# Performance work log

Measured on AMD Instinct MI355X. Metric: run time of the kernel, lower is better.

Reference implementation:

```python
import jax, jax.numpy as jnp
import numpy as np

OUTPUT_SIZE = 16384          # number of map units (must be a perfect square)
SIDE = 128.0                 # sqrt(OUTPUT_SIZE)
SIGMA = 2.0                  # neighbourhood std-dev (non-trainable weight in original)
B, D = 2048, 256


def setup_inputs() -> dict:
    key = jax.random.key(0)
    k1, k2 = jax.random.split(key)
    x = jax.random.normal(k1, (B, D), dtype=jnp.float32)
    kernel = jax.random.normal(k2, (D, OUTPUT_SIZE), dtype=jnp.float32) * 0.1
    return {"x": x, "kernel": kernel}


def _grid_coords():
    # 2D coordinates of each flattened map unit: unit k -> (k // side, k % side)
    idx = jnp.arange(OUTPUT_SIZE, dtype=jnp.float32)
    return jnp.floor(idx / SIDE), jnp.mod(idx, SIDE)  # each (size,)


def reference(x, kernel):
    # Squared Euclidean distance of every sample to every prototype: (B, size).
    # Same math as tf.norm(x[:, :, None] - kernel[None])**2, expressed as a GEMM.
    norms2 = (jnp.sum(x * x, axis=1, keepdims=True)
              - 2.0 * (x @ kernel)
              + jnp.sum(kernel * kernel, axis=0, keepdims=True))
    norms2 = jnp.maximum(norms2, 0.0)

    # Winner-take-all unit per sample, mapped to 2D grid coordinates.
    wta = jnp.argmin(norms2, axis=1).astype(jnp.float32)        # (B,)
    mean_r = jnp.floor(wta / SIDE)                               # (B,)
    mean_c = jnp.mod(wta, SIDE)                                  # (B,)

    # Gaussian neighbourhood over the 2D grid, flattened: (B, size).
    gr, gc = _grid_coords()
    dr = gr[None, :] - mean_r[:, None]
    dc = gc[None, :] - mean_c[:, None]
    radials = jnp.exp(-0.5 / (SIGMA * SIGMA) * (dr * dr + dc * dc))

    return radials * norms2
```

## Files before the change

### kernel.cpp

```cpp
#include <hip/hip_runtime.h>
#include <hip/hip_fp16.h>

#define OUTN 16384
#define BATCH 2048
#define DIM   256

typedef _Float16 half8 __attribute__((ext_vector_type(8)));
typedef float    floatx4 __attribute__((ext_vector_type(4)));
typedef unsigned long long u64;

__device__ __forceinline__ void gl2lds16(const void* g, void* l) {
    __builtin_amdgcn_global_load_lds(
        (const __attribute__((address_space(1))) void*)g,
        (__attribute__((address_space(3))) void*)l, 16, 0, 0);
}

__device__ __forceinline__ u64 packkey(float v, int col) {
    unsigned u = __float_as_uint(v);
    u = (u & 0x80000000u) ? ~u : (u | 0x80000000u);
    return ((u64)u << 32) | (unsigned)col;
}
__device__ __forceinline__ float unpackval(u64 p) {
    unsigned u = (unsigned)(p >> 32);
    u = (u & 0x80000000u) ? (u & 0x7fffffffu) : ~u;
    return __uint_as_float(u);
}

__global__ __launch_bounds__(256) void prep_all(
        const float* __restrict__ x, const float* __restrict__ kern,
        _Float16* __restrict__ xh, float* __restrict__ rown,
        _Float16* __restrict__ kT, float* __restrict__ colnp) {
    int blk = blockIdx.x, t = threadIdx.x;
    if (blk < 512) {
        __shared__ float tile[64][65];
        __shared__ float npart[4][64];
        int tx = t & 63, ty = t >> 6;
        int j0 = (blk >> 1) * 64;
        int dhalf = blk & 1, dbase = dhalf * 128;
        float nrm = 0.f;
        for (int pc = 0; pc < 2; pc++) {
            int dc = dbase + pc * 64;
            __syncthreads();
            for (int it = 0; it < 16; it++) {
                int d = dc + ty + it * 4;
                float v = kern[(size_t)d * OUTN + j0 + tx];
                tile[ty + it * 4][tx] = v;
                nrm = fmaf(v, v, nrm);
            }
            __syncthreads();
            for (int c = t; c < 512; c += 256) {
                int j = c >> 3, o8 = (c & 7) * 8;
                half8 h;
                for (int u = 0; u < 8; u++) h[u] = (_Float16)tile[o8 + u][j];
                *(half8*)&kT[(size_t)(j0 + j) * DIM + dc + o8] = h;
            }
        }
        npart[ty][tx] = nrm;
        __syncthreads();
        if (t < 64)
            colnp[(size_t)dhalf * OUTN + j0 + t] =
                npart[0][t] + npart[1][t] + npart[2][t] + npart[3][t];
    } else {
        int b = blk - 512;
        float v = x[b * DIM + t];
        xh[b * DIM + t] = (_Float16)v;
        float s = v * v;
        for (int off = 32; off; off >>= 1) s += __shfl_down(s, off, 64);
        __shared__ float wsum[4];
        if ((t & 63) == 0) wsum[t >> 6] = s;
        __syncthreads();
        if (t == 0) rown[b] = wsum[0] + wsum[1] + wsum[2] + wsum[3];
    }
}

template <bool NF16>
__global__ __launch_bounds__(256) void gemm_norms(
        const _Float16* __restrict__ xh, const _Float16* __restrict__ kT,
        const float* __restrict__ rown, const float* __restrict__ colnp,
        void* __restrict__ n2out, u64* __restrict__ blockcand) {
    __shared__ __align__(16) char smem[32768];
    _Float16* As = (_Float16*)smem;
    _Float16* Bs = (_Float16*)(smem + 16384);
    u64* cand = (u64*)smem;
    int tid  = threadIdx.x;
    int col0 = blockIdx.x * 128;
    int row0 = blockIdx.y * 128;
    int wid = tid >> 6, lane = tid & 63;
    int wr = wid >> 1, wc = wid & 1;
    int l15 = lane & 15, l4 = lane >> 4;
    int xh7 = l15 & 7;

    floatx4 acc[4][4];
    for (int i = 0; i < 4; i++)
        for (int j = 0; j < 4; j++)
            acc[i][j] = (floatx4){0.f, 0.f, 0.f, 0.f};

    for (int kt = 0; kt < 4; kt++) {
        int k0 = kt * 64;
        for (int it = 0; it < 4; it++) {
            int chunk = it * 256 + tid;
            int r = chunk >> 3, gg = chunk & 7;
            int ksw = (gg ^ (r & 7)) * 8;
            gl2lds16(&xh[(size_t)(row0 + r) * DIM + k0 + ksw], &As[chunk * 8]);
            gl2lds16(&kT[(size_t)(col0 + r) * DIM + k0 + ksw], &Bs[chunk * 8]);
        }
        __syncthreads();
        for (int s = 0; s < 2; s++) {
            int g = s * 4 + l4;
            int sw = (g ^ xh7) * 8;
            half8 af[4], bf[4];
            for (int i = 0; i < 4; i++)
                af[i] = *(half8*)&As[(wr * 64 + i * 16 + l15) * 64 + sw];
            for (int j = 0; j < 4; j++)
                bf[j] = *(half8*)&Bs[(wc * 64 + j * 16 + l15) * 64 + sw];
            for (int i = 0; i < 4; i++)
                for (int j = 0; j < 4; j++)
                    acc[i][j] = __builtin_amdgcn_mfma_f32_16x16x32_f16(
                        af[i], bf[j], acc[i][j], 0, 0, 0);
        }
        __syncthreads();
    }

    float cn[4]; int oc[4];
    for (int j = 0; j < 4; j++) {
        oc[j] = col0 + wc * 64 + j * 16 + l15;
        cn[j] = colnp[oc[j]] + colnp[OUTN + oc[j]];
    }
    for (int i = 0; i < 4; i++) {
        for (int r = 0; r < 4; r++) {
            int row_l = wr * 64 + i * 16 + l4 * 4 + r;
            int orow  = row0 + row_l;
            float rn = rown[orow];
            u64 best = ~0ull;
            for (int j = 0; j < 4; j++) {
                float val = rn + cn[j] - 2.0f * acc[i][j][r];
                size_t oi = (size_t)orow * OUTN + oc[j];
                if (NF16) ((_Float16*)n2out)[oi] = (_Float16)val;
                else      ((float*)n2out)[oi]    = val;
                u64 p = packkey(val, oc[j]);
                if (p < best) best = p;
            }
            cand[row_l * 32 + wc * 16 + l15] = best;
        }
    }
    __syncthreads();
    if (tid < 128) {
        u64 m1 = ~0ull, m2 = ~0ull;
        for (int s = 0; s < 32; s++) {
            u64 v = cand[tid * 32 + s];
            if (v < m1) { m2 = m1; m1 = v; }
            else if (v < m2) { m2 = v; }
        }
        size_t base = (size_t)(row0 + tid) * 256 + blockIdx.x * 2;
        blockcand[base]     = m1;
        blockcand[base + 1] = m2;
    }
}

template <bool NF16>
__global__ __launch_bounds__(256) void refine_finalize(
        const u64* __restrict__ blockcand, const float* __restrict__ x,
        const float* __restrict__ kern, const float* __restrict__ colnp,
        const void* __restrict__ n2in, float* __restrict__ out) {
    int b = blockIdx.x, t = threadIdx.x;
    __shared__ float xrow[DIM];
    __shared__ u64 red[256];
    xrow[t] = x[b * DIM + t];
    u64 e = blockcand[(size_t)b * 256 + t];
    red[t] = e;
    __syncthreads();
    for (int off = 128; off; off >>= 1) {
        if (t < off) { u64 o = red[t + off]; if (o < red[t]) red[t] = o; }
        __syncthreads();
    }
    float minv = unpackval(red[0]);
    __syncthreads();

    float ve = unpackval(e);
    u64 p = ~0ull;
    if (ve <= minv + 0.125f) {
        int j = (int)(e & 0xffffffffu);
        float dot = 0.f;
        for (int d = 0; d < DIM; d++)
            dot = fmaf(xrow[d], kern[(size_t)d * OUTN + j], dot);
        p = packkey((colnp[j] + colnp[OUTN + j]) - 2.0f * dot, j);
    }
    red[t] = p;
    __syncthreads();
    for (int off = 128; off; off >>= 1) {
        if (t < off) { u64 o = red[t + off]; if (o < red[t]) red[t] = o; }
        __syncthreads();
    }
    int w = (int)(red[0] & 0xffffffffu);
    int wrr = w >> 7, wcc = w & 127;

    const _Float16* r16 = (const _Float16*)n2in + (size_t)b * OUTN;
    const float*    r32 = (const float*)n2in    + (size_t)b * OUTN;
    float* rowp = out + (size_t)b * OUTN;
    for (int it = 0; it < 16; it++) {
        int idx4 = it * 256 + t;
        int j0 = idx4 * 4;
        int r  = j0 >> 7, c0 = j0 & 127;
        int dr = r - wrr, drsq = dr * dr;
        float4 res;
        {
            int dc = c0 - wcc;     int d2 = drsq + dc * dc;
            float v = (d2 <= 720) ? (NF16 ? (float)r16[j0]     : r32[j0])     : 0.f;
            res.x = (d2 <= 720) ? __expf(-0.125f * (float)d2) * fmaxf(v, 0.f) : 0.f;
        }
        {
            int dc = c0 + 1 - wcc; int d2 = drsq + dc * dc;
            float v = (d2 <= 720) ? (NF16 ? (float)r16[j0 + 1] : r32[j0 + 1]) : 0.f;
            res.y = (d2 <= 720) ? __expf(-0.125f * (float)d2) * fmaxf(v, 0.f) : 0.f;
        }
        {
            int dc = c0 + 2 - wcc; int d2 = drsq + dc * dc;
            float v = (d2 <= 720) ? (NF16 ? (float)r16[j0 + 2] : r32[j0 + 2]) : 0.f;
            res.z = (d2 <= 720) ? __expf(-0.125f * (float)d2) * fmaxf(v, 0.f) : 0.f;
        }
        {
            int dc = c0 + 3 - wcc; int d2 = drsq + dc * dc;
            float v = (d2 <= 720) ? (NF16 ? (float)r16[j0 + 3] : r32[j0 + 3]) : 0.f;
            res.w = (d2 <= 720) ? __expf(-0.125f * (float)d2) * fmaxf(v, 0.f) : 0.f;
        }
        ((float4*)rowp)[idx4] = res;
    }
}

extern "C" void kernel_launch(void* const* d_in, const int* in_sizes, int n_in,
                              void* d_out, int out_size, void* d_ws, size_t ws_size,
                              hipStream_t stream) {
    const float* x    = (const float*)d_in[0];
    const float* kern = (const float*)d_in[1];
    float* out = (float*)d_out;
    char* ws = (char*)d_ws;

    _Float16* xh   = (_Float16*)(ws);
    _Float16* kT   = (_Float16*)(ws + (1u << 20));
    float*   colnp = (float*)(ws + (9u << 20));
    float*   rown  = (float*)(ws + (9u << 20) + (128u << 10));
    u64* blockcand = (u64*)(ws + (10u << 20));
    void*    n2h   = (void*)(ws + (14u << 20));
    bool f16path = ws_size >= ((size_t)78 << 20);

    prep_all<<<2560, 256, 0, stream>>>(x, kern, xh, rown, kT, colnp);
    if (f16path) {
        gemm_norms<true><<<dim3(OUTN / 128, BATCH / 128), 256, 0, stream>>>(
            xh, kT, rown, colnp, n2h, blockcand);
        refine_finalize<true><<<BATCH, 256, 0, stream>>>(
            blockcand, x, kern, colnp, n2h, out);
    } else {
        gemm_norms<false><<<dim3(OUTN / 128, BATCH / 128), 256, 0, stream>>>(
            xh, kT, rown, colnp, (void*)out, blockcand);
        refine_finalize<false><<<BATCH, 256, 0, stream>>>(
            blockcand, x, kern, colnp, (const void*)out, out);
    }
}
```

Before: 202.1 us.

## Recompute GEMM in second pass to fuse Gaussian epilogue and drop norms buffer

Splits the work into a candidate-only GEMM, a refine step that writes just the winner index per row, and a second GEMM that recomputes the distances and applies the separable Gaussian weight in its epilogue, staging tiles in LDS for coalesced float4 output stores. This removes the write and read of the full intermediate distance matrix (fp16 or fp32) and the separate finalize pass, at the cost of running the fp16 MFMA GEMM twice. The refine step now reads a new transposed fp32 copy of the kernel built in prep, so its dot product uses contiguous rows instead of strided columns; that copy adds extra write traffic in prep. The Gaussian factor is now evaluated over the full map for every output instead of being cut off beyond a distance threshold.

```diff
diff --git a/kernel.cpp b/kernel.cpp
--- a/kernel.cpp
+++ b/kernel.cpp
@@ -29,7 +29,8 @@
 __global__ __launch_bounds__(256) void prep_all(
         const float* __restrict__ x, const float* __restrict__ kern,
         _Float16* __restrict__ xh, float* __restrict__ rown,
-        _Float16* __restrict__ kT, float* __restrict__ colnp) {
+        _Float16* __restrict__ kT, float* __restrict__ kT32,
+        float* __restrict__ colnp) {
     int blk = blockIdx.x, t = threadIdx.x;
     if (blk < 512) {
         __shared__ float tile[64][65];
@@ -51,8 +52,15 @@
             for (int c = t; c < 512; c += 256) {
                 int j = c >> 3, o8 = (c & 7) * 8;
                 half8 h;
-                for (int u = 0; u < 8; u++) h[u] = (_Float16)tile[o8 + u][j];
+                float4 f0, f1;
+                float vv[8];
+                for (int u = 0; u < 8; u++) { vv[u] = tile[o8 + u][j]; h[u] = (_Float16)vv[u]; }
+                f0 = make_float4(vv[0], vv[1], vv[2], vv[3]);
+                f1 = make_float4(vv[4], vv[5], vv[6], vv[7]);
                 *(half8*)&kT[(size_t)(j0 + j) * DIM + dc + o8] = h;
+                float* kp = &kT32[(size_t)(j0 + j) * DIM + dc + o8];
+                *(float4*)kp = f0;
+                *(float4*)(kp + 4) = f1;
             }
         }
         npart[ty][tx] = nrm;
@@ -73,11 +81,9 @@
     }
 }
 
-template <bool NF16>
-__global__ __launch_bounds__(256) void gemm_norms(
+__global__ __launch_bounds__(256) void gemm_cand(
         const _Float16* __restrict__ xh, const _Float16* __restrict__ kT,
-        const float* __restrict__ rown, const float* __restrict__ colnp,
-        void* __restrict__ n2out, u64* __restrict__ blockcand) {
+        const float* __restrict__ colnp, u64* __restrict__ blockcand) {
     __shared__ __align__(16) char smem[32768];
     _Float16* As = (_Float16*)smem;
     _Float16* Bs = (_Float16*)(smem + 16384);
@@ -129,15 +135,9 @@
     for (int i = 0; i < 4; i++) {
         for (int r = 0; r < 4; r++) {
             int row_l = wr * 64 + i * 16 + l4 * 4 + r;
-            int orow  = row0 + row_l;
-            float rn = rown[orow];
             u64 best = ~0ull;
             for (int j = 0; j < 4; j++) {
-                float val = rn + cn[j] - 2.0f * acc[i][j][r];
-                size_t oi = (size_t)orow * OUTN + oc[j];
-                if (NF16) ((_Float16*)n2out)[oi] = (_Float16)val;
-                else      ((float*)n2out)[oi]    = val;
-                u64 p = packkey(val, oc[j]);
+                u64 p = packkey(cn[j] - 2.0f * acc[i][j][r], oc[j]);
                 if (p < best) best = p;
             }
             cand[row_l * 32 + wc * 16 + l15] = best;
@@ -157,11 +157,10 @@
     }
 }
 
-template <bool NF16>
-__global__ __launch_bounds__(256) void refine_finalize(
+__global__ __launch_bounds__(256) void refine(
         const u64* __restrict__ blockcand, const float* __restrict__ x,
-        const float* __restrict__ kern, const float* __restrict__ colnp,
-        const void* __restrict__ n2in, float* __restrict__ out) {
+        const float* __restrict__ kT32, const float* __restrict__ colnp,
+        int* __restrict__ wta) {
     int b = blockIdx.x, t = threadIdx.x;
     __shared__ float xrow[DIM];
     __shared__ u64 red[256];
@@ -176,13 +175,13 @@
     float minv = unpackval(red[0]);
     __syncthreads();
 
-    float ve = unpackval(e);
     u64 p = ~0ull;
-    if (ve <= minv + 0.125f) {
+    if (unpackval(e) <= minv + 0.125f) {
         int j = (int)(e & 0xffffffffu);
+        const float* kr = kT32 + (size_t)j * DIM;
         float dot = 0.f;
         for (int d = 0; d < DIM; d++)
-            dot = fmaf(xrow[d], kern[(size_t)d * OUTN + j], dot);
+            dot = fmaf(xrow[d], kr[d], dot);
         p = packkey((colnp[j] + colnp[OUTN + j]) - 2.0f * dot, j);
     }
     red[t] = p;
@@ -191,39 +190,97 @@
         if (t < off) { u64 o = red[t + off]; if (o < red[t]) red[t] = o; }
         __syncthreads();
     }
-    int w = (int)(red[0] & 0xffffffffu);
-    int wrr = w >> 7, wcc = w & 127;
-
-    const _Float16* r16 = (const _Float16*)n2in + (size_t)b * OUTN;
-    const float*    r32 = (const float*)n2in    + (size_t)b * OUTN;
-    float* rowp = out + (size_t)b * OUTN;
-    for (int it = 0; it < 16; it++) {
-        int idx4 = it * 256 + t;
-        int j0 = idx4 * 4;
-        int r  = j0 >> 7, c0 = j0 & 127;
-        int dr = r - wrr, drsq = dr * dr;
-        float4 res;
-        {
-            int dc = c0 - wcc;     int d2 = drsq + dc * dc;
-            float v = (d2 <= 720) ? (NF16 ? (float)r16[j0]     : r32[j0])     : 0.f;
-            res.x = (d2 <= 720) ? __expf(-0.125f * (float)d2) * fmaxf(v, 0.f) : 0.f;
-        }
-        {
-            int dc = c0 + 1 - wcc; int d2 = drsq + dc * dc;
-            float v = (d2 <= 720) ? (NF16 ? (float)r16[j0 + 1] : r32[j0 + 1]) : 0.f;
-            res.y = (d2 <= 720) ? __expf(-0.125f * (float)d2) * fmaxf(v, 0.f) : 0.f;
-        }
-        {
-            int dc = c0 + 2 - wcc; int d2 = drsq + dc * dc;
-            float v = (d2 <= 720) ? (NF16 ? (float)r16[j0 + 2] : r32[j0 + 2]) : 0.f;
-            res.z = (d2 <= 720) ? __expf(-0.125f * (float)d2) * fmaxf(v, 0.f) : 0.f;
-        }
-        {
-            int dc = c0 + 3 - wcc; int d2 = drsq + dc * dc;
-            float v = (d2 <= 720) ? (NF16 ? (float)r16[j0 + 3] : r32[j0 + 3]) : 0.f;
-            res.w = (d2 <= 720) ? __expf(-0.125f * (float)d2) * fmaxf(v, 0.f) : 0.f;
-        }
-        ((float4*)rowp)[idx4] = res;
+    if (t == 0) wta[b] = (int)(red[0] & 0xffffffffu);
+}
+
+__global__ __launch_bounds__(256) void gemm_out(
+        const _Float16* __restrict__ xh, const _Float16* __restrict__ kT,
+        const float* __restrict__ rown, const float* __restrict__ colnp,
+        const int* __restrict__ wta, float* __restrict__ out) {
+    __shared__ __align__(16) char smem[32768];
+    _Float16* As = (_Float16*)smem;
+    _Float16* Bs = (_Float16*)(smem + 16384);
+    float* buf = (float*)smem;
+    __shared__ int   wtal[128];
+    __shared__ float rnl[128];
+    __shared__ float colf[128];
+    int tid  = threadIdx.x;
+    int col0 = blockIdx.x * 128;
+    int row0 = blockIdx.y * 128;
+    int wid = tid >> 6, lane = tid & 63;
+    int wr = wid >> 1, wc = wid & 1;
+    int l15 = lane & 15, l4 = lane >> 4;
+    int xh7 = l15 & 7;
+
+    if (tid < 128) {
+        wtal[tid] = wta[row0 + tid];
+        rnl[tid]  = rown[row0 + tid];
+        colf[tid] = __expf(-0.125f * (float)(tid * tid));
+    }
+
+    floatx4 acc[4][4];
+    for (int i = 0; i < 4; i++)
+        for (int j = 0; j < 4; j++)
+            acc[i][j] = (floatx4){0.f, 0.f, 0.f, 0.f};
+
+    for (int kt = 0; kt < 4; kt++) {
+        int k0 = kt * 64;
+        for (int it = 0; it < 4; it++) {
+            int chunk = it * 256 + tid;
+            int r = chunk >> 3, gg = chunk & 7;
+            int ksw = (gg ^ (r & 7)) * 8;
+            gl2lds16(&xh[(size_t)(row0 + r) * DIM + k0 + ksw], &As[chunk * 8]);
+            gl2lds16(&kT[(size_t)(col0 + r) * DIM + k0 + ksw], &Bs[chunk * 8]);
+        }
+        __syncthreads();
+        for (int s = 0; s < 2; s++) {
+            int g = s * 4 + l4;
+            int sw = (g ^ xh7) * 8;
+            half8 af[4], bf[4];
+            for (int i = 0; i < 4; i++)
+                af[i] = *(half8*)&As[(wr * 64 + i * 16 + l15) * 64 + sw];
+            for (int j = 0; j < 4; j++)
+                bf[j] = *(half8*)&Bs[(wc * 64 + j * 16 + l15) * 64 + sw];
+            for (int i = 0; i < 4; i++)
+                for (int j = 0; j < 4; j++)
+                    acc[i][j] = __builtin_amdgcn_mfma_f32_16x16x32_f16(
+                        af[i], bf[j], acc[i][j], 0, 0, 0);
+        }
+        __syncthreads();
+    }
+
+    float cn[4]; int gcj[4];
+    for (int j = 0; j < 4; j++) {
+        int oc = col0 + wc * 64 + j * 16 + l15;
+        cn[j]  = colnp[oc] + colnp[OUTN + oc];
+        gcj[j] = oc & 127;
+    }
+    for (int h = 0; h < 2; h++) {
+        if (wr == h) {
+            for (int i = 0; i < 4; i++) {
+                for (int r = 0; r < 4; r++) {
+                    int row_l = i * 16 + l4 * 4 + r;
+                    float rn = rnl[h * 64 + row_l];
+                    int w = wtal[h * 64 + row_l];
+                    int dr = blockIdx.x - (w >> 7); dr = dr < 0 ? -dr : dr;
+                    float rowf = colf[dr];
+                    int wcc = w & 127;
+                    for (int j = 0; j < 4; j++) {
+                        int dc = gcj[j] - wcc; dc = dc < 0 ? -dc : dc;
+                        float val = rn + cn[j] - 2.0f * acc[i][j][r];
+                        buf[row_l * 128 + wc * 64 + j * 16 + l15] =
+                            rowf * colf[dc] * fmaxf(val, 0.f);
+                    }
+                }
+            }
+        }
+        __syncthreads();
+        for (int q = tid; q < 2048; q += 256) {
+            int rr = q >> 5, cc = (q & 31) * 4;
+            *(float4*)&out[(size_t)(row0 + h * 64 + rr) * OUTN + col0 + cc] =
+                *(float4*)&buf[rr * 128 + cc];
+        }
+        __syncthreads();
     }
 }
 
@@ -237,22 +294,14 @@
 
     _Float16* xh   = (_Float16*)(ws);
     _Float16* kT   = (_Float16*)(ws + (1u << 20));
-    float*   colnp = (float*)(ws + (9u << 20));
-    float*   rown  = (float*)(ws + (9u << 20) + (128u << 10));
-    u64* blockcand = (u64*)(ws + (10u << 20));
-    void*    n2h   = (void*)(ws + (14u << 20));
-    bool f16path = ws_size >= ((size_t)78 << 20);
-
-    prep_all<<<2560, 256, 0, stream>>>(x, kern, xh, rown, kT, colnp);
-    if (f16path) {
-        gemm_norms<true><<<dim3(OUTN / 128, BATCH / 128), 256, 0, stream>>>(
-            xh, kT, rown, colnp, n2h, blockcand);
-        refine_finalize<true><<<BATCH, 256, 0, stream>>>(
-            blockcand, x, kern, colnp, n2h, out);
-    } else {
-        gemm_norms<false><<<dim3(OUTN / 128, BATCH / 128), 256, 0, stream>>>(
-            xh, kT, rown, colnp, (void*)out, blockcand);
-        refine_finalize<false><<<BATCH, 256, 0, stream>>>(
-            blockcand, x, kern, colnp, (const void*)out, out);
-    }
-}
+    float*    kT32 = (float*)(ws + (9u << 20));
+    float*   colnp = (float*)(ws + (25u << 20));
+    float*    rown = (float*)(ws + (25u << 20) + (128u << 10));
+    int*       wta = (int*)(ws + (25u << 20) + (136u << 10));
+    u64* blockcand = (u64*)(ws + (26u << 20));
+
+    prep_all<<<2560, 256, 0, stream>>>(x, kern, xh, rown, kT, kT32, colnp);
+    gemm_cand<<<dim3(OUTN / 128, BATCH / 128), 256, 0, stream>>>(xh, kT, colnp, blockcand);
+    refine<<<BATCH, 256, 0, stream>>>(blockcand, x, kT32, colnp, wta);
+    gemm_out<<<dim3(OUTN / 128, BATCH / 128), 256, 0, stream>>>(xh, kT, rown, colnp, wta, out);
+}
```

Measured after the change: 218.3 us. 8.0% more time.
